# Kernel optimization log

Measured on AMD Instinct MI355X. Metric: run time of the kernel, lower is better.

The kernel has to match this reference:

```python
import jax, jax.numpy as jnp
import numpy as np


def setup_inputs() -> dict:
    key = jax.random.key(0)
    ks = jax.random.split(key, 9)
    B, C, H, W, D = 2, 64, 64, 64, 16
    Cq = C // 8
    return {
        "x2d": jax.random.normal(ks[0], (B, C, H, W, D), jnp.float32),
        "x3d": jax.random.normal(ks[1], (B, C, H, W, D), jnp.float32),
        "Wq": jax.random.normal(ks[2], (Cq, C), jnp.float32) * 0.05,
        "bq": jax.random.normal(ks[3], (Cq,), jnp.float32) * 0.05,
        "Wk": jax.random.normal(ks[4], (Cq, C), jnp.float32) * 0.05,
        "bk": jax.random.normal(ks[5], (Cq,), jnp.float32) * 0.05,
        "Wv": jax.random.normal(ks[6], (C, C), jnp.float32) * 0.05,
        "bv": jax.random.normal(ks[7], (C,), jnp.float32) * 0.05,
        "gamma": jax.random.normal(ks[8], (1,), jnp.float32),
    }


def reference(x2d, x3d, Wq, bq, Wk, bk, Wv, bv, gamma):
    # x2d/x3d: (B, C, H, W, D) -> permute to (B, C, D, H, W)
    xp = jnp.transpose(x2d, (0, 1, 4, 2, 3))
    B, C, D, H, W = xp.shape
    N = H * W

    # 1x1x1 Conv3d == channel contraction
    q = jnp.einsum('oc,bcdhw->bodhw', Wq, xp) + bq[None, :, None, None, None]
    k = jnp.einsum('oc,bcdhw->bodhw', Wk, xp) + bk[None, :, None, None, None]
    v = jnp.einsum('oc,bcdhw->bodhw', Wv, xp) + bv[None, :, None, None, None]

    # fold depth into feature dim; attention over N = H*W positions
    pq = q.reshape(B, -1, N)                  # (B, Cq*D, N)
    pk = k.reshape(B, -1, N)                  # (B, Cq*D, N)
    energy = jnp.einsum('bcn,bcm->bnm', pq, pk)   # (B, N, N)
    attn = jax.nn.softmax(energy, axis=-1)

    pv = v.reshape(B, -1, N)                  # (B, C*D, N)
    # out[b,c,n] = sum_m pv[b,c,m] * attn[b,n,m]
    out = jnp.einsum('bcm,bnm->bcn', pv, attn)
    out = out.reshape(B, C, D, H, W)
    out = jnp.transpose(out, (0, 1, 3, 4, 2))  # back to (B, C, H, W, D)
    return gamma * out + x3d
```

## Files before the change

### kernel.cpp

```cpp
#include <hip/hip_runtime.h>
#include <hip/hip_bf16.h>

typedef __attribute__((ext_vector_type(8))) short short8;
typedef __attribute__((ext_vector_type(8))) __bf16 bf16x8;
typedef __attribute__((ext_vector_type(4))) float f32x4;

#define N_   4096
#define CQD  128
#define CVD  1024
#define PLD  136

static __device__ __forceinline__ unsigned short f2bf(float f) {
    union { float f; unsigned int u; } cv; cv.f = f;
    unsigned int u = cv.u;
    u += 0x7fffu + ((u >> 16) & 1u);
    return (unsigned short)(u >> 16);
}

static __device__ __forceinline__ f32x4 mfma16(bf16x8 a, bf16x8 b, f32x4 c) {
    return __builtin_amdgcn_mfma_f32_16x16x32_bf16(a, b, c, 0, 0, 0);
}

__global__ __launch_bounds__(256) void proj_kernel(
    const float* __restrict__ x2d,
    const float* __restrict__ Wq, const float* __restrict__ bq,
    const float* __restrict__ Wk, const float* __restrict__ bk,
    const float* __restrict__ Wv, const float* __restrict__ bv,
    unsigned short* __restrict__ Qb, unsigned short* __restrict__ Kb,
    unsigned short* __restrict__ PV)
{
    const int t  = threadIdx.x;
    const int blk = blockIdx.x;
    const int b  = blk >> 8;
    const int n0 = (blk & 255) << 4;
    const int n  = t & 15;
    const int dd = t >> 4;

    const float* xb = x2d + ((size_t)b * 64 * N_ + (size_t)(n0 + n)) * 16 + dd;
    float xr[64];
#pragma unroll
    for (int c = 0; c < 64; ++c) xr[c] = xb[(size_t)c * (N_ * 16)];

    unsigned short* pvb = PV + (size_t)b * CVD * N_;
    for (int j = 0; j < 64; ++j) {
        float acc = bv[j];
#pragma unroll
        for (int c = 0; c < 64; ++c) acc += Wv[j * 64 + c] * xr[c];
        pvb[(size_t)(j * 16 + dd) * N_ + n0 + n] = f2bf(acc);
    }
    unsigned short* qb = Qb + (size_t)b * N_ * CQD;
    unsigned short* kb = Kb + (size_t)b * N_ * CQD;
    for (int j = 0; j < 8; ++j) {
        float aq = bq[j], ak = bk[j];
#pragma unroll
        for (int c = 0; c < 64; ++c) {
            float xv = xr[c];
            aq += Wq[j * 64 + c] * xv;
            ak += Wk[j * 64 + c] * xv;
        }
        qb[(size_t)(n0 + n) * CQD + j * 16 + dd] = f2bf(aq);
        kb[(size_t)(n0 + n) * CQD + j * 16 + dd] = f2bf(ak);
    }
}

__global__ __launch_bounds__(512, 2) void attn_kernel(
    const unsigned short* __restrict__ Qb, const unsigned short* __restrict__ Kb,
    const unsigned short* __restrict__ PV,
    const float* __restrict__ x3d, const float* __restrict__ gamma_p,
    float* __restrict__ outp)
{
    __shared__ unsigned short p_lds[2][64][PLD];
    __shared__ float red[64];

    const int t  = threadIdx.x;
    const int w  = t >> 6;
    const int l  = t & 63;
    const int lo = l & 15;
    const int hi = l >> 4;

    const int id    = blockIdx.x;
    const int combo = (id >> 1) & 3;
    const int chalf = combo & 1;
    const int b     = combo >> 1;
    const int xl    = ((id >> 3) << 1) | (id & 1);
    const int n0    = xl << 6;
    const int cw    = (chalf << 9) + (w << 6);
    const int g     = w >> 2;
    const int msel  = w & 3;

    const unsigned short* qp  = Qb + (size_t)b * N_ * CQD;
    const unsigned short* kp  = Kb + (size_t)b * N_ * CQD;
    const unsigned short* pvp = PV + (size_t)b * CVD * N_;

    bf16x8 qf[2][4];
#pragma unroll
    for (int ns = 0; ns < 2; ++ns)
#pragma unroll
        for (int kk = 0; kk < 4; ++kk)
            qf[ns][kk] = *reinterpret_cast<const bf16x8*>(
                qp + (size_t)(n0 + g * 32 + ns * 16 + lo) * CQD + kk * 32 + hi * 8);

    f32x4 acc[4][4];
#pragma unroll
    for (int i = 0; i < 4; ++i)
#pragma unroll
        for (int j = 0; j < 4; ++j) acc[i][j] = (f32x4){0.f, 0.f, 0.f, 0.f};
    float rs[8];
#pragma unroll
    for (int i = 0; i < 8; ++i) rs[i] = 0.f;

    if (t < 64) red[t] = 0.f;

    for (int it = 0; it < 32; ++it) {
        const int m0  = it << 7;
        const int buf = it & 1;
        const int mc  = m0 + (msel << 5);

        bf16x8 kf[2][4];
#pragma unroll
        for (int ms = 0; ms < 2; ++ms)
#pragma unroll
            for (int kk = 0; kk < 4; ++kk)
                kf[ms][kk] = *reinterpret_cast<const bf16x8*>(
                    kp + (size_t)(mc + ms * 16 + lo) * CQD + kk * 32 + hi * 8);
        f32x4 e[2][2];
#pragma unroll
        for (int ns = 0; ns < 2; ++ns)
#pragma unroll
            for (int ms = 0; ms < 2; ++ms) {
                f32x4 ee = (f32x4){0.f, 0.f, 0.f, 0.f};
#pragma unroll
                for (int kk = 0; kk < 4; ++kk) ee = mfma16(qf[ns][kk], kf[ms][kk], ee);
                e[ns][ms] = ee;
            }
#pragma unroll
        for (int ns = 0; ns < 2; ++ns)
#pragma unroll
            for (int ms = 0; ms < 2; ++ms)
#pragma unroll
                for (int r = 0; r < 4; ++r) {
                    float p = __expf(e[ns][ms][r]);
                    rs[ns * 4 + r] += p;
                    p_lds[buf][g * 32 + ns * 16 + hi * 4 + r][(msel << 5) + ms * 16 + lo] = f2bf(p);
                }
        __syncthreads();

#pragma unroll
        for (int kk = 0; kk < 4; ++kk) {
            bf16x8 af[4];
#pragma unroll
            for (int ns = 0; ns < 4; ++ns)
                af[ns] = *reinterpret_cast<const bf16x8*>(&p_lds[buf][ns * 16 + lo][kk * 32 + hi * 8]);
            bf16x8 bvv[4];
#pragma unroll
            for (int cs = 0; cs < 4; ++cs)
                bvv[cs] = *reinterpret_cast<const bf16x8*>(
                    pvp + (size_t)(cw + cs * 16 + lo) * N_ + m0 + kk * 32 + hi * 8);
#pragma unroll
            for (int ns = 0; ns < 4; ++ns)
#pragma unroll
                for (int cs = 0; cs < 4; ++cs)
                    acc[ns][cs] = mfma16(af[ns], bvv[cs], acc[ns][cs]);
        }
    }

#pragma unroll
    for (int i = 0; i < 8; ++i) {
        float v = rs[i];
        v += __shfl_xor(v, 1);
        v += __shfl_xor(v, 2);
        v += __shfl_xor(v, 4);
        v += __shfl_xor(v, 8);
        rs[i] = v;
    }
    if (lo == 0) {
#pragma unroll
        for (int ns = 0; ns < 2; ++ns)
#pragma unroll
            for (int r = 0; r < 4; ++r)
                atomicAdd(&red[g * 32 + ns * 16 + hi * 4 + r], rs[ns * 4 + r]);
    }
    __syncthreads();

    const float gmv = gamma_p[0];
    const float* x3p = x3d + (size_t)b * 64 * N_ * 16;
    float* op        = outp + (size_t)b * 64 * N_ * 16;
#pragma unroll
    for (int ns = 0; ns < 4; ++ns) {
        float rinv[4];
#pragma unroll
        for (int r = 0; r < 4; ++r) rinv[r] = 1.0f / red[ns * 16 + hi * 4 + r];
#pragma unroll
        for (int cs = 0; cs < 4; ++cs) {
            const int cp = cw + cs * 16 + lo;
            const size_t base = (size_t)(cp >> 4) * (N_ * 16) + (size_t)(cp & 15);
#pragma unroll
            for (int r = 0; r < 4; ++r) {
                const size_t idx = base + (size_t)(n0 + ns * 16 + hi * 4 + r) * 16;
                op[idx] = gmv * acc[ns][cs][r] * rinv[r] + x3p[idx];
            }
        }
    }
}

extern "C" void kernel_launch(void* const* d_in, const int* in_sizes, int n_in,
                              void* d_out, int out_size, void* d_ws, size_t ws_size,
                              hipStream_t stream)
{
    const float* x2d = (const float*)d_in[0];
    const float* x3d = (const float*)d_in[1];
    const float* Wq  = (const float*)d_in[2];
    const float* bq  = (const float*)d_in[3];
    const float* Wk  = (const float*)d_in[4];
    const float* bk  = (const float*)d_in[5];
    const float* Wv  = (const float*)d_in[6];
    const float* bv  = (const float*)d_in[7];
    const float* gm  = (const float*)d_in[8];

    char* ws = (char*)d_ws;
    unsigned short* Qb = (unsigned short*)ws;
    unsigned short* Kb = (unsigned short*)(ws + (2u << 20));
    unsigned short* PV = (unsigned short*)(ws + (4u << 20));

    proj_kernel<<<512, 256, 0, stream>>>(x2d, Wq, bq, Wk, bk, Wv, bv, Qb, Kb, PV);
    attn_kernel<<<256, 512, 0, stream>>>(Qb, Kb, PV, x3d, gm, (float*)d_out);
}
```

Before: 382.8 us.

## Coalesce projection loads via LDS-staged V stores and split attention channels finer

The projection kernel now assigns threads to contiguous (n,d) columns, so x2d reads are coalesced. V results are staged through shared memory and written to PV as 16-byte vectors instead of scattered 2-byte stores. The attention kernel splits the value channels into quarters instead of halves, doubling the grid to 512 blocks with fewer accumulators per wave and a launch-bounds hint of 4 blocks per SM. The finer split raises occupancy but doubles the recomputation of QK energies and exp across channel groups.

```diff
diff --git a/kernel.cpp b/kernel.cpp
--- a/kernel.cpp
+++ b/kernel.cpp
@@ -7,7 +7,6 @@
 
 #define N_   4096
 #define CQD  128
-#define CVD  1024
 #define PLD  136
 
 static __device__ __forceinline__ unsigned short f2bf(float f) {
@@ -29,27 +28,25 @@
     unsigned short* __restrict__ Qb, unsigned short* __restrict__ Kb,
     unsigned short* __restrict__ PV)
 {
-    const int t  = threadIdx.x;
-    const int blk = blockIdx.x;
-    const int b  = blk >> 8;
-    const int n0 = (blk & 255) << 4;
-    const int n  = t & 15;
-    const int dd = t >> 4;
-
-    const float* xb = x2d + ((size_t)b * 64 * N_ + (size_t)(n0 + n)) * 16 + dd;
+    __shared__ unsigned short vlds[64][16][24];
+
+    const int t    = threadIdx.x;
+    const int blk  = blockIdx.x;
+    const int b    = blk >> 8;
+    const int nblk = blk & 255;
+    const int col  = (nblk << 8) + t;
+    const int n    = col >> 4;
+    const int dd   = col & 15;
+    const int nl   = n & 15;
+
+    const float* xb = x2d + (size_t)b * 64 * 65536 + col;
     float xr[64];
 #pragma unroll
-    for (int c = 0; c < 64; ++c) xr[c] = xb[(size_t)c * (N_ * 16)];
-
-    unsigned short* pvb = PV + (size_t)b * CVD * N_;
-    for (int j = 0; j < 64; ++j) {
-        float acc = bv[j];
-#pragma unroll
-        for (int c = 0; c < 64; ++c) acc += Wv[j * 64 + c] * xr[c];
-        pvb[(size_t)(j * 16 + dd) * N_ + n0 + n] = f2bf(acc);
-    }
-    unsigned short* qb = Qb + (size_t)b * N_ * CQD;
-    unsigned short* kb = Kb + (size_t)b * N_ * CQD;
+    for (int c = 0; c < 64; ++c) xr[c] = xb[(size_t)c * 65536];
+
+    unsigned short* qb = Qb + (size_t)b * N_ * CQD + (size_t)n * CQD + dd;
+    unsigned short* kb = Kb + (size_t)b * N_ * CQD + (size_t)n * CQD + dd;
+#pragma unroll 2
     for (int j = 0; j < 8; ++j) {
         float aq = bq[j], ak = bk[j];
 #pragma unroll
@@ -58,12 +55,31 @@
             aq += Wq[j * 64 + c] * xv;
             ak += Wk[j * 64 + c] * xv;
         }
-        qb[(size_t)(n0 + n) * CQD + j * 16 + dd] = f2bf(aq);
-        kb[(size_t)(n0 + n) * CQD + j * 16 + dd] = f2bf(ak);
-    }
-}
-
-__global__ __launch_bounds__(512, 2) void attn_kernel(
+        qb[j * 16] = f2bf(aq);
+        kb[j * 16] = f2bf(ak);
+    }
+
+#pragma unroll 4
+    for (int j = 0; j < 64; ++j) {
+        float acc = bv[j];
+#pragma unroll
+        for (int c = 0; c < 64; ++c) acc += Wv[j * 64 + c] * xr[c];
+        vlds[j][dd][nl] = f2bf(acc);
+    }
+    __syncthreads();
+
+    unsigned short* pvb = PV + (size_t)b * 1024 * N_ + (size_t)(nblk << 4);
+#pragma unroll
+    for (int rr = 0; rr < 4; ++rr) {
+        const int r = (rr << 8) + t;
+        const short8 v0 = *reinterpret_cast<const short8*>(&vlds[r >> 4][r & 15][0]);
+        const short8 v1 = *reinterpret_cast<const short8*>(&vlds[r >> 4][r & 15][8]);
+        *reinterpret_cast<short8*>(pvb + (size_t)r * N_)     = v0;
+        *reinterpret_cast<short8*>(pvb + (size_t)r * N_ + 8) = v1;
+    }
+}
+
+__global__ __launch_bounds__(512, 4) void attn_kernel(
     const unsigned short* __restrict__ Qb, const unsigned short* __restrict__ Kb,
     const unsigned short* __restrict__ PV,
     const float* __restrict__ x3d, const float* __restrict__ gamma_p,
@@ -79,18 +95,18 @@
     const int hi = l >> 4;
 
     const int id    = blockIdx.x;
-    const int combo = (id >> 1) & 3;
-    const int chalf = combo & 1;
-    const int b     = combo >> 1;
-    const int xl    = ((id >> 3) << 1) | (id & 1);
-    const int n0    = xl << 6;
-    const int cw    = (chalf << 9) + (w << 6);
+    const int combo = id & 7;
+    const int ntile = id >> 3;
+    const int b     = combo >> 2;
+    const int cq    = combo & 3;
+    const int n0    = ntile << 6;
+    const int cw    = (cq << 8) + (w << 5);
     const int g     = w >> 2;
     const int msel  = w & 3;
 
     const unsigned short* qp  = Qb + (size_t)b * N_ * CQD;
     const unsigned short* kp  = Kb + (size_t)b * N_ * CQD;
-    const unsigned short* pvp = PV + (size_t)b * CVD * N_;
+    const unsigned short* pvp = PV + (size_t)b * 1024 * N_;
 
     bf16x8 qf[2][4];
 #pragma unroll
@@ -100,11 +116,11 @@
             qf[ns][kk] = *reinterpret_cast<const bf16x8*>(
                 qp + (size_t)(n0 + g * 32 + ns * 16 + lo) * CQD + kk * 32 + hi * 8);
 
-    f32x4 acc[4][4];
+    f32x4 acc[4][2];
 #pragma unroll
     for (int i = 0; i < 4; ++i)
 #pragma unroll
-        for (int j = 0; j < 4; ++j) acc[i][j] = (f32x4){0.f, 0.f, 0.f, 0.f};
+        for (int j = 0; j < 2; ++j) acc[i][j] = (f32x4){0.f, 0.f, 0.f, 0.f};
     float rs[8];
 #pragma unroll
     for (int i = 0; i < 8; ++i) rs[i] = 0.f;
@@ -116,33 +132,30 @@
         const int buf = it & 1;
         const int mc  = m0 + (msel << 5);
 
-        bf16x8 kf[2][4];
-#pragma unroll
-        for (int ms = 0; ms < 2; ++ms)
+#pragma unroll
+        for (int ms = 0; ms < 2; ++ms) {
+            bf16x8 kf[4];
 #pragma unroll
             for (int kk = 0; kk < 4; ++kk)
-                kf[ms][kk] = *reinterpret_cast<const bf16x8*>(
+                kf[kk] = *reinterpret_cast<const bf16x8*>(
                     kp + (size_t)(mc + ms * 16 + lo) * CQD + kk * 32 + hi * 8);
-        f32x4 e[2][2];
-#pragma unroll
-        for (int ns = 0; ns < 2; ++ns)
-#pragma unroll
-            for (int ms = 0; ms < 2; ++ms) {
-                f32x4 ee = (f32x4){0.f, 0.f, 0.f, 0.f};
-#pragma unroll
-                for (int kk = 0; kk < 4; ++kk) ee = mfma16(qf[ns][kk], kf[ms][kk], ee);
-                e[ns][ms] = ee;
+            f32x4 e0 = (f32x4){0.f, 0.f, 0.f, 0.f};
+            f32x4 e1 = (f32x4){0.f, 0.f, 0.f, 0.f};
+#pragma unroll
+            for (int kk = 0; kk < 4; ++kk) {
+                e0 = mfma16(qf[0][kk], kf[kk], e0);
+                e1 = mfma16(qf[1][kk], kf[kk], e1);
             }
 #pragma unroll
-        for (int ns = 0; ns < 2; ++ns)
-#pragma unroll
-            for (int ms = 0; ms < 2; ++ms)
-#pragma unroll
-                for (int r = 0; r < 4; ++r) {
-                    float p = __expf(e[ns][ms][r]);
-                    rs[ns * 4 + r] += p;
-                    p_lds[buf][g * 32 + ns * 16 + hi * 4 + r][(msel << 5) + ms * 16 + lo] = f2bf(p);
-                }
+            for (int r = 0; r < 4; ++r) {
+                float p0 = __expf(e0[r]);
+                float p1 = __expf(e1[r]);
+                rs[r]     += p0;
+                rs[4 + r] += p1;
+                p_lds[buf][g * 32 + hi * 4 + r][(msel << 5) + ms * 16 + lo]      = f2bf(p0);
+                p_lds[buf][g * 32 + 16 + hi * 4 + r][(msel << 5) + ms * 16 + lo] = f2bf(p1);
+            }
+        }
         __syncthreads();
 
 #pragma unroll
@@ -151,15 +164,15 @@
 #pragma unroll
             for (int ns = 0; ns < 4; ++ns)
                 af[ns] = *reinterpret_cast<const bf16x8*>(&p_lds[buf][ns * 16 + lo][kk * 32 + hi * 8]);
-            bf16x8 bvv[4];
-#pragma unroll
-            for (int cs = 0; cs < 4; ++cs)
+            bf16x8 bvv[2];
+#pragma unroll
+            for (int cs = 0; cs < 2; ++cs)
                 bvv[cs] = *reinterpret_cast<const bf16x8*>(
                     pvp + (size_t)(cw + cs * 16 + lo) * N_ + m0 + kk * 32 + hi * 8);
 #pragma unroll
             for (int ns = 0; ns < 4; ++ns)
 #pragma unroll
-                for (int cs = 0; cs < 4; ++cs)
+                for (int cs = 0; cs < 2; ++cs)
                     acc[ns][cs] = mfma16(af[ns], bvv[cs], acc[ns][cs]);
         }
     }
@@ -191,7 +204,7 @@
 #pragma unroll
         for (int r = 0; r < 4; ++r) rinv[r] = 1.0f / red[ns * 16 + hi * 4 + r];
 #pragma unroll
-        for (int cs = 0; cs < 4; ++cs) {
+        for (int cs = 0; cs < 2; ++cs) {
             const int cp = cw + cs * 16 + lo;
             const size_t base = (size_t)(cp >> 4) * (N_ * 16) + (size_t)(cp & 15);
 #pragma unroll
@@ -223,5 +236,5 @@
     unsigned short* PV = (unsigned short*)(ws + (4u << 20));
 
     proj_kernel<<<512, 256, 0, stream>>>(x2d, Wq, bq, Wk, bk, Wv, bv, Qb, Kb, PV);
-    attn_kernel<<<256, 512, 0, stream>>>(Qb, Kb, PV, x3d, gm, (float*)d_out);
-}
+    attn_kernel<<<512, 512, 0, stream>>>(Qb, Kb, PV, x3d, gm, (float*)d_out);
+}
```

New measurement: 442.7 us. 15.6% more time.
